# Optimization experiments

Hardware: AMD Instinct MI355X
Metric: run time of the kernel (lower is better)

## Reference

```python
import math
import jax, jax.numpy as jnp
import numpy as np


def _skew(X, pad_value):
    # shift every row i one step right relative to row i-1: [B,M,L] -> [B,M,M+L]
    B, M, L = X.shape
    X = jnp.pad(X, ((0, 0), (0, 0), (0, M + 1)), constant_values=pad_value)
    X = X.reshape(B, -1)[:, :-M]
    return X.reshape(B, M, M + L)


def _unskew(X):
    # reverse of _skew: [B,M,M+L] -> [B,M,L]
    B, M, ML = X.shape
    L = ML - M
    X = X.reshape(B, -1)
    X = jnp.pad(X, ((0, 0), (0, M)))
    X = X.reshape(B, M, M + L + 1)
    return X[:, :, :L]


def setup_inputs() -> dict:
    key0 = jax.random.key(0)
    k1, k2, k3, k4 = jax.random.split(key0, 4)
    BH, M, D = 64, 1024, 64          # batch*heads, block len, head dim
    L = 1024                          # attn_span
    return {
        "query": jax.random.normal(k1, (BH, M, D), dtype=jnp.float32),
        "key": jax.random.normal(k2, (BH, M + L, D), dtype=jnp.float32),
        "value": jax.random.normal(k3, (BH, M + L, D), dtype=jnp.float32),
        "key_pe": jax.random.normal(k4, (1, D, L), dtype=jnp.float32),
    }


def reference(query, key, value, key_pe):
    hidden_size = query.shape[-1]
    # content scores: [BH, M, M+L] -> banded [BH, M, L]
    attn_cont = _unskew(jnp.matmul(query, jnp.swapaxes(key, -1, -2)))
    # relative position scores: [BH, M, L] (key_pe broadcasts over batch)
    attn_pos = jnp.matmul(query, key_pe)
    attn = (attn_cont + attn_pos) / math.sqrt(hidden_size)
    attn = jax.nn.softmax(attn, axis=-1)
    # dropout p=0.0 -> identity
    attn_skew = _skew(attn, 0.0)          # [BH, M, M+L]
    out = jnp.matmul(attn_skew, value)    # [BH, M, D]
    return out
```

## Files before the change

### kernel.cpp

```cpp
#include <hip/hip_runtime.h>
#include <hip/hip_bf16.h>


typedef __attribute__((ext_vector_type(8))) short bf16x8;
typedef __attribute__((ext_vector_type(4))) short bf16x4;
typedef __attribute__((ext_vector_type(4))) float f32x4;

#define BHN   64
#define MQ    1024
#define DH    64
#define LS    1024
#define NKEY  2048
#define NT    18
#define NPE   16

#define SZ_PE  ((size_t)LS * DH * 2)
#define OFF_K  SZ_PE
#define SZ_K   ((size_t)BHN * NKEY * DH * 2)
#define OFF_V  (OFF_K + SZ_K)
#define SZ_V   ((size_t)BHN * DH * NKEY * 2)
#define WS_NEED (OFF_V + SZ_V)

#define SCL_LOG2E 0.18033688011112042f

__device__ __forceinline__ short f2bf(float f) {
  unsigned u = __float_as_uint(f);
  u += 0x7FFFu + ((u >> 16) & 1u);
  return (short)(u >> 16);
}
__device__ __forceinline__ float bf2f(short s) {
  return __uint_as_float(((unsigned)(unsigned short)s) << 16);
}

#if defined(__has_builtin)
#if __has_builtin(__builtin_amdgcn_cvt_pk_bf16_f32)
#define HAVE_CVT_PK 1
#endif
#if __has_builtin(__builtin_amdgcn_exp2f)
#define HAVE_EXP2 1
#endif
#endif

__device__ __forceinline__ float fast_exp2(float x) {
#ifdef HAVE_EXP2
  return __builtin_amdgcn_exp2f(x);
#else
  return __builtin_exp2f(x);
#endif
}

__device__ __forceinline__ unsigned pk2(float a, float b) {
#ifdef HAVE_CVT_PK
  auto r = __builtin_amdgcn_cvt_pk_bf16_f32(a, b);
  unsigned u;
  __builtin_memcpy(&u, &r, 4);
  return u;
#else
  return (unsigned)(unsigned short)f2bf(a) | ((unsigned)(unsigned short)f2bf(b) << 16);
#endif
}
__device__ __forceinline__ bf16x4 mk4(unsigned a, unsigned b) {
  union { unsigned u[2]; bf16x4 v; } z;
  z.u[0] = a; z.u[1] = b;
  return z.v;
}
__device__ __forceinline__ bf16x8 mk8(unsigned a, unsigned b, unsigned c, unsigned d) {
  union { unsigned u[4]; bf16x8 v; } z;
  z.u[0] = a; z.u[1] = b; z.u[2] = c; z.u[3] = d;
  return z.v;
}

__global__ __launch_bounds__(256)
void prep_fused(const float* __restrict__ pe, const float* __restrict__ K,
                const float* __restrict__ V, short* __restrict__ peT,
                short* __restrict__ Kb, short* __restrict__ Vb) {
  __shared__ short st[64 * 68];
  const int bx = blockIdx.x;
  if (bx < 256) {
    const int idx = bx * 256 + threadIdx.x;
    const int rel = idx >> 6, d = idx & 63;
    peT[rel * 64 + (((d >> 3) ^ (rel & 7)) * 8) + (d & 7)] = f2bf(pe[d * LS + rel]);
  } else if (bx < 2304) {
    const size_t i = ((size_t)(bx - 256) * 256 + threadIdx.x) * 16;
    const int row = (int)(i >> 6);
    const int c16 = (int)(i & 63);
    const float4 f0 = *(const float4*)(K + i);
    const float4 f1 = *(const float4*)(K + i + 4);
    const float4 f2 = *(const float4*)(K + i + 8);
    const float4 f3 = *(const float4*)(K + i + 12);
    const bf16x8 b0 = mk8(pk2(f0.x, f0.y), pk2(f0.z, f0.w), pk2(f1.x, f1.y), pk2(f1.z, f1.w));
    const bf16x8 b1 = mk8(pk2(f2.x, f2.y), pk2(f2.z, f2.w), pk2(f3.x, f3.y), pk2(f3.z, f3.w));
    const int s7 = row & 7;
    short* dst = Kb + (size_t)row * 64;
    *(bf16x8*)&dst[(((c16 >> 3))     ^ s7) * 8] = b0;
    *(bf16x8*)&dst[(((c16 >> 3) + 1) ^ s7) * 8] = b1;
  } else {
    const int b  = bx - 2304;
    const int bh = b >> 5, jt = b & 31;
    {
      const int r = threadIdx.x >> 2, cb = (threadIdx.x & 3) * 16;
      const float* src = V + ((size_t)bh * NKEY + jt * 64 + r) * DH + cb;
#pragma unroll
      for (int c = 0; c < 16; c += 8) {
        float4 f0 = *(const float4*)(src + c);
        float4 f1 = *(const float4*)(src + c + 4);
        *(bf16x8*)&st[r * 68 + cb + c] =
            mk8(pk2(f0.x, f0.y), pk2(f0.z, f0.w), pk2(f1.x, f1.y), pk2(f1.z, f1.w));
      }
    }
    __syncthreads();
    {
      const int d = threadIdx.x >> 2, kapb = (threadIdx.x & 3) * 16;
      __attribute__((aligned(16))) short tmp[16];
#pragma unroll
      for (int j = 0; j < 16; ++j) {
        const int kap = kapb + j;
        const int k   = (kap & 3) * 16 + (kap >> 2);
        tmp[j] = st[k * 68 + d];
      }
      short* dst = Vb + ((size_t)bh * DH + d) * NKEY + jt * 64 + kapb;
      *(bf16x8*)dst       = *(bf16x8*)&tmp[0];
      *(bf16x8*)(dst + 8) = *(bf16x8*)&tmp[8];
    }
  }
}

__device__ __forceinline__ void softmax_band(
    const f32x4* cs, const f32x4* cur, const f32x4& prev,
    float (&l_acc)[4], short* sPA, const int rowbase, const int tt,
    const int w, const int li, const int quad) {
#pragma unroll
  for (int r = 0; r < 4; ++r) {
    const int e       = li - quad * 4 - r;
    const bool ge     = (e >= 0);
    const int srcLane = quad * 16 + (e & 15);
    const float shm = __shfl(prev[r], srcLane);
    const unsigned pk01 = pk2(cur[0][r], cur[1][r]);
    const unsigned pk23 = pk2(cur[2][r], cur[3][r]);
    const unsigned s01 = (unsigned)__shfl((int)pk01, srcLane);
    const unsigned s23 = (unsigned)__shfl((int)pk23, srcLane);
    const float sh0 = bf2f((short)(s01 & 0xffffu));
    const float sh1 = bf2f((short)(s01 >> 16));
    const float sh2 = bf2f((short)(s23 & 0xffffu));
    const float sh3 = bf2f((short)(s23 >> 16));
    const float pos0 = ge ? sh0 : shm;
    const float pos1 = ge ? sh1 : sh0;
    const float pos2 = ge ? sh2 : sh1;
    const float pos3 = ge ? sh3 : sh2;
    float p0 = fast_exp2(cs[0][r] + pos0);
    float p1 = fast_exp2(cs[1][r] + pos1);
    float p2 = fast_exp2(cs[2][r] + pos2);
    float p3 = fast_exp2(cs[3][r] + pos3);
    if (tt == 0) {
      p0 = (0 > w || (0 == w && ge)) ? p0 : 0.f;
      p1 = (1 > w || (1 == w && ge)) ? p1 : 0.f;
      p2 = (2 > w || (2 == w && ge)) ? p2 : 0.f;
      p3 = (3 > w || (3 == w && ge)) ? p3 : 0.f;
    } else if (tt == 16) {
      p0 = (0 < w || (0 == w && !ge)) ? p0 : 0.f;
      p1 = (1 < w || (1 == w && !ge)) ? p1 : 0.f;
      p2 = (2 < w || (2 == w && !ge)) ? p2 : 0.f;
      p3 = (3 < w || (3 == w && !ge)) ? p3 : 0.f;
    } else if ((unsigned)tt > 16u) {
      p0 = 0.f; p1 = 0.f; p2 = 0.f; p3 = 0.f;
    }
    l_acc[r] += (p0 + p1) + (p2 + p3);
    const int rowA = rowbase + w * 16 + quad * 4 + r;
    const bf16x4 pkv = mk4(pk2(p0, p1), pk2(p2, p3));
    *(bf16x4*)&sPA[rowA * 64 + (((li >> 1) ^ (rowA & 7)) * 8) + (li & 1) * 4] = pkv;
  }
}

template <bool PRECONV>
__global__ __launch_bounds__(256, 2)
void seq_attn_kernel(const float* __restrict__ Qf, const float* __restrict__ Kf,
                     const float* __restrict__ Vf, const short* __restrict__ peT,
                     const short* __restrict__ Kb, const short* __restrict__ Vb,
                     float* __restrict__ Out) {
  __shared__ short sK[64 * 64];
  __shared__ short sPE[4 * 64 * 64];
  __shared__ short sV[64 * 64];
  __shared__ short sPA[128 * 64];

  const int tid  = threadIdx.x;
  const int w    = tid >> 6;
  const int lane = tid & 63;
  const int li   = lane & 15;
  const int quad = lane >> 4;
  const int linear = blockIdx.y * 8 + blockIdx.x;
  const int within = linear >> 3;
  const int bh     = (linear & 7) * 8 + (within >> 3);
  const int i0     = (within & 7) * 128;
  const int rbase  = w * 16 + quad * 4;

  bf16x8 aq0[2], aq1[2];
#pragma unroll
  for (int g = 0; g < 2; ++g) {
    const float* qp = Qf + (size_t)((bh * MQ + i0 + g * 64 + w * 16 + li) * DH) + quad * 8;
#pragma unroll
    for (int ks = 0; ks < 2; ++ks) {
      float4 f0 = *(const float4*)(qp + ks * 32);
      float4 f1 = *(const float4*)(qp + ks * 32 + 4);
      f0.x *= SCL_LOG2E; f0.y *= SCL_LOG2E; f0.z *= SCL_LOG2E; f0.w *= SCL_LOG2E;
      f1.x *= SCL_LOG2E; f1.y *= SCL_LOG2E; f1.z *= SCL_LOG2E; f1.w *= SCL_LOG2E;
      const bf16x8 v = mk8(pk2(f0.x, f0.y), pk2(f0.z, f0.w), pk2(f1.x, f1.y), pk2(f1.z, f1.w));
      if (g == 0) aq0[ks] = v; else aq1[ks] = v;
    }
  }

  float l0[4] = {0.f, 0.f, 0.f, 0.f};
  float l1[4] = {0.f, 0.f, 0.f, 0.f};
  f32x4 acco0[4], acco1[4];
#pragma unroll
  for (int nt = 0; nt < 4; ++nt) {
    acco0[nt] = (f32x4){0.f, 0.f, 0.f, 0.f};
    acco1[nt] = (f32x4){0.f, 0.f, 0.f, 0.f};
  }
  f32x4 prev0 = (f32x4){0.f, 0.f, 0.f, 0.f};
  f32x4 prev1 = (f32x4){0.f, 0.f, 0.f, 0.f};

  bf16x8 pfK0, pfK1, pfP0, pfP1, pfV0, pfV1;
  const short *pK, *pP, *pV0, *pV1;
  if constexpr (PRECONV) {
    pK = Kb + ((size_t)bh * NKEY + i0) * DH + tid * 8 + 1024;
    pP = peT + tid * 8 + 1024;
    const int d0 = tid >> 3;
    const int g0 = (tid & 7) ^ (d0 & 7);
    pV0 = Vb + ((size_t)bh * DH + d0) * NKEY + i0 + g0 * 8;
    pV1 = pV0 + (size_t)32 * NKEY;
    pfK0 = *(const bf16x8*)(pK - 1024);
    pfK1 = *(const bf16x8*)(pK + 1024);
    pfP0 = *(const bf16x8*)(pP - 1024);
    pfP1 = *(const bf16x8*)(pP + 1024);
    pfV0 = *(const bf16x8*)(pV0);
    pfV1 = *(const bf16x8*)(pV1);
    pK += 4096; pP += 4096; pV0 += 64; pV1 += 64;
  }

  for (int t = 0; t < NT; ++t) {
    if constexpr (PRECONV) {
      asm volatile("s_waitcnt lgkmcnt(0)" ::: "memory");
      __builtin_amdgcn_sched_barrier(0);
      __builtin_amdgcn_s_barrier();
      __builtin_amdgcn_sched_barrier(0);
      *(bf16x8*)&sK[tid * 8]        = pfK0;
      *(bf16x8*)&sK[tid * 8 + 2048] = pfK1;
      if (t < NPE) {
        short* ped = sPE + (size_t)(t & 3) * 4096;
        *(bf16x8*)&ped[tid * 8]        = pfP0;
        *(bf16x8*)&ped[tid * 8 + 2048] = pfP1;
      }
      *(bf16x8*)&sV[tid * 8]        = pfV0;
      *(bf16x8*)&sV[tid * 8 + 2048] = pfV1;
      if (t + 1 < NT) {
        pfK0 = *(const bf16x8*)(pK - 1024);
        pfK1 = *(const bf16x8*)(pK + 1024);
        pfV0 = *(const bf16x8*)(pV0);
        pfV1 = *(const bf16x8*)(pV1);
        pK += 4096; pV0 += 64; pV1 += 64;
        if (t + 1 < NPE) {
          pfP0 = *(const bf16x8*)(pP - 1024);
          pfP1 = *(const bf16x8*)(pP + 1024);
          pP += 4096;
        }
      }
      asm volatile("s_waitcnt lgkmcnt(0)" ::: "memory");
      __builtin_amdgcn_sched_barrier(0);
      __builtin_amdgcn_s_barrier();
      __builtin_amdgcn_sched_barrier(0);
    } else {
      __syncthreads();
      const int j0 = i0 + t * 64;
      {
        const int srow = tid >> 2, lx = tid & 3, sdb = lx * 16;
        const float* src = Kf + (size_t)(bh * NKEY + j0 + srow) * DH + sdb;
        const float4 a0 = *(const float4*)(src + 0);
        const float4 a1 = *(const float4*)(src + 4);
        const float4 a2 = *(const float4*)(src + 8);
        const float4 a3 = *(const float4*)(src + 12);
        const bf16x8 b0 = mk8(pk2(a0.x, a0.y), pk2(a0.z, a0.w), pk2(a1.x, a1.y), pk2(a1.z, a1.w));
        const bf16x8 b1 = mk8(pk2(a2.x, a2.y), pk2(a2.z, a2.w), pk2(a3.x, a3.y), pk2(a3.z, a3.w));
        const int s7 = srow & 7;
        *(bf16x8*)&sK[srow * 64 + (((2 * lx)     ^ s7) * 8)] = b0;
        *(bf16x8*)&sK[srow * 64 + (((2 * lx + 1) ^ s7) * 8)] = b1;
      }
      {
        const int vdb = (tid & 15) * 4, vkb = (tid >> 4) * 4;
        const float* src = Vf + (size_t)(bh * NKEY + j0 + vkb) * DH + vdb;
#pragma unroll
        for (int m = 0; m < 4; ++m) {
          const float4 rr = *(const float4*)(src + m * DH);
          const int k   = vkb + m;
          const int kap = (k & 15) * 4 + (k >> 4);
#pragma unroll
          for (int jj = 0; jj < 4; ++jj) {
            const int d = vdb + jj;
            const float fv = (jj == 0) ? rr.x : (jj == 1) ? rr.y : (jj == 2) ? rr.z : rr.w;
            sV[d * 64 + (((kap >> 3) ^ (d & 7)) * 8) + (kap & 7)] = f2bf(fv);
          }
        }
      }
      if (t < NPE) {
        const short* src = peT + (size_t)t * 64 * 64;
        short* db = sPE + (size_t)(t & 3) * 4096;
        *(bf16x8*)&db[tid * 16]     = *(const bf16x8*)(src + tid * 16);
        *(bf16x8*)&db[tid * 16 + 8] = *(const bf16x8*)(src + tid * 16 + 8);
      }
      __syncthreads();
    }

    f32x4 cur0[4], cur1[4];
    __builtin_amdgcn_s_setprio(1);
#pragma unroll
    for (int m = 0; m < 4; ++m) {
      const int colIdx = 4 * t - w + m;
      const int base = ((colIdx >> 2) & 3) * 4096 + ((colIdx & 3) * 16 + li) * 64;
      f32x4 c = (f32x4){0.f, 0.f, 0.f, 0.f};
#pragma unroll
      for (int ks = 0; ks < 2; ++ks) {
        const int gs = (((ks * 4 + quad) ^ (li & 7)) * 8);
        const bf16x8 b = *(bf16x8*)&sPE[base + gs];
        c = __builtin_amdgcn_mfma_f32_16x16x32_bf16(aq0[ks], b, c, 0, 0, 0);
      }
      cur0[m] = c;
    }
#pragma unroll
    for (int m = 0; m < 4; ++m) {
      const int colIdx = 4 * t - w + m - 4;
      const int base = ((colIdx >> 2) & 3) * 4096 + ((colIdx & 3) * 16 + li) * 64;
      f32x4 c = (f32x4){0.f, 0.f, 0.f, 0.f};
#pragma unroll
      for (int ks = 0; ks < 2; ++ks) {
        const int gs = (((ks * 4 + quad) ^ (li & 7)) * 8);
        const bf16x8 b = *(bf16x8*)&sPE[base + gs];
        c = __builtin_amdgcn_mfma_f32_16x16x32_bf16(aq1[ks], b, c, 0, 0, 0);
      }
      cur1[m] = c;
    }

    f32x4 cs0[4], cs1[4];
#pragma unroll
    for (int nt = 0; nt < 4; ++nt) {
      f32x4 c0 = (f32x4){0.f, 0.f, 0.f, 0.f};
      f32x4 c1 = (f32x4){0.f, 0.f, 0.f, 0.f};
#pragma unroll
      for (int ks = 0; ks < 2; ++ks) {
        const int gs = (((ks * 4 + quad) ^ (li & 7)) * 8);
        const bf16x8 b = *(bf16x8*)&sK[(nt * 16 + li) * 64 + gs];
        c0 = __builtin_amdgcn_mfma_f32_16x16x32_bf16(aq0[ks], b, c0, 0, 0, 0);
        c1 = __builtin_amdgcn_mfma_f32_16x16x32_bf16(aq1[ks], b, c1, 0, 0, 0);
      }
      cs0[nt] = c0; cs1[nt] = c1;
    }
    __builtin_amdgcn_s_setprio(0);

    softmax_band(cs0, cur0, prev0, l0, sPA, 0,  t,     w, li, quad);
    softmax_band(cs1, cur1, prev1, l1, sPA, 64, t - 1, w, li, quad);
    prev0 = cur0[3];
    prev1 = cur1[3];

    __builtin_amdgcn_s_setprio(1);
#pragma unroll
    for (int ks = 0; ks < 2; ++ks) {
      const int rA0 = w * 16 + li;
      const int rA1 = rA0 + 64;
      const bf16x8 ap0 = *(bf16x8*)&sPA[rA0 * 64 + (((ks * 4 + quad) ^ (rA0 & 7)) * 8)];
      const bf16x8 ap1 = *(bf16x8*)&sPA[rA1 * 64 + (((ks * 4 + quad) ^ (rA1 & 7)) * 8)];
#pragma unroll
      for (int nt = 0; nt < 4; ++nt) {
        const int d  = nt * 16 + li;
        const int gs = (((ks * 4 + quad) ^ (d & 7)) * 8);
        const bf16x8 bv = *(bf16x8*)&sV[d * 64 + gs];
        acco0[nt] = __builtin_amdgcn_mfma_f32_16x16x32_bf16(ap0, bv, acco0[nt], 0, 0, 0);
        acco1[nt] = __builtin_amdgcn_mfma_f32_16x16x32_bf16(ap1, bv, acco1[nt], 0, 0, 0);
      }
    }
    __builtin_amdgcn_s_setprio(0);
  }

#pragma unroll
  for (int r = 0; r < 4; ++r) {
    float l = l0[r];
    l += __shfl_xor(l, 1);
    l += __shfl_xor(l, 2);
    l += __shfl_xor(l, 4);
    l += __shfl_xor(l, 8);
    const float inv = 1.0f / l;
#pragma unroll
    for (int nt = 0; nt < 4; ++nt) {
      Out[(size_t)(bh * MQ + i0 + rbase + r) * DH + nt * 16 + li] = acco0[nt][r] * inv;
    }
  }
#pragma unroll
  for (int r = 0; r < 4; ++r) {
    float l = l1[r];
    l += __shfl_xor(l, 1);
    l += __shfl_xor(l, 2);
    l += __shfl_xor(l, 4);
    l += __shfl_xor(l, 8);
    const float inv = 1.0f / l;
#pragma unroll
    for (int nt = 0; nt < 4; ++nt) {
      Out[(size_t)(bh * MQ + i0 + 64 + rbase + r) * DH + nt * 16 + li] = acco1[nt][r] * inv;
    }
  }
}

extern "C" void kernel_launch(void* const* d_in, const int* in_sizes, int n_in,
                              void* d_out, int out_size, void* d_ws, size_t ws_size,
                              hipStream_t stream) {
  const float* q  = (const float*)d_in[0];
  const float* k  = (const float*)d_in[1];
  const float* v  = (const float*)d_in[2];
  const float* pe = (const float*)d_in[3];
  float* out = (float*)d_out;
  short* peT = (short*)d_ws;
  short* Kb  = (short*)((char*)d_ws + OFF_K);
  short* Vb  = (short*)((char*)d_ws + OFF_V);
  const bool preconv = ws_size >= WS_NEED;

  dim3 grid(8, BHN);
  if (preconv) {
    prep_fused<<<4352, 256, 0, stream>>>(pe, k, v, peT, Kb, Vb);
    seq_attn_kernel<true><<<grid, 256, 0, stream>>>(q, k, v, peT, Kb, Vb, out);
  } else {
    prep_fused<<<256, 256, 0, stream>>>(pe, k, v, peT, Kb, Vb);
    seq_attn_kernel<false><<<grid, 256, 0, stream>>>(q, k, v, peT, Kb, Vb, out);
  }
}
```

Before: 175.4 us.

## Shrink shared memory to fit three blocks per CU by reusing sK for P

```diff
diff --git a/kernel.cpp b/kernel.cpp
--- a/kernel.cpp
+++ b/kernel.cpp
@@ -127,7 +127,7 @@
 
 __device__ __forceinline__ void softmax_band(
     const f32x4* cs, const f32x4* cur, const f32x4& prev,
-    float (&l_acc)[4], short* sPA, const int rowbase, const int tt,
+    float (&l_acc)[4], short* dst, const int tt,
     const int w, const int li, const int quad) {
 #pragma unroll
   for (int r = 0; r < 4; ++r) {
@@ -165,22 +165,22 @@
       p0 = 0.f; p1 = 0.f; p2 = 0.f; p3 = 0.f;
     }
     l_acc[r] += (p0 + p1) + (p2 + p3);
-    const int rowA = rowbase + w * 16 + quad * 4 + r;
+    const int rowA = w * 16 + quad * 4 + r;
     const bf16x4 pkv = mk4(pk2(p0, p1), pk2(p2, p3));
-    *(bf16x4*)&sPA[rowA * 64 + (((li >> 1) ^ (rowA & 7)) * 8) + (li & 1) * 4] = pkv;
+    *(bf16x4*)&dst[rowA * 64 + (((li >> 1) ^ (rowA & 7)) * 8) + (li & 1) * 4] = pkv;
   }
 }
 
 template <bool PRECONV>
-__global__ __launch_bounds__(256, 2)
+__global__ __launch_bounds__(256, 3)
 void seq_attn_kernel(const float* __restrict__ Qf, const float* __restrict__ Kf,
                      const float* __restrict__ Vf, const short* __restrict__ peT,
                      const short* __restrict__ Kb, const short* __restrict__ Vb,
                      float* __restrict__ Out) {
   __shared__ short sK[64 * 64];
-  __shared__ short sPE[4 * 64 * 64];
+  __shared__ short sPE[3 * 64 * 64];
   __shared__ short sV[64 * 64];
-  __shared__ short sPA[128 * 64];
+  __shared__ short sPA[64 * 64];
 
   const int tid  = threadIdx.x;
   const int w    = tid >> 6;
@@ -218,6 +218,11 @@
   }
   f32x4 prev0 = (f32x4){0.f, 0.f, 0.f, 0.f};
   f32x4 prev1 = (f32x4){0.f, 0.f, 0.f, 0.f};
+
+  int peRow[4];
+#pragma unroll
+  for (int m = 0; m < 4; ++m) peRow[m] = (((m - w) & 3) * 16 + li) * 64;
+  int sCur = 0, sPrev = 2, sPrev2 = 1;
 
   bf16x8 pfK0, pfK1, pfP0, pfP1, pfV0, pfV1;
   const short *pK, *pP, *pV0, *pV1;
@@ -246,7 +251,7 @@
       *(bf16x8*)&sK[tid * 8]        = pfK0;
       *(bf16x8*)&sK[tid * 8 + 2048] = pfK1;
       if (t < NPE) {
-        short* ped = sPE + (size_t)(t & 3) * 4096;
+        short* ped = sPE + (size_t)sCur * 4096;
         *(bf16x8*)&ped[tid * 8]        = pfP0;
         *(bf16x8*)&ped[tid * 8 + 2048] = pfP1;
       }
@@ -302,7 +307,7 @@
       }
       if (t < NPE) {
         const short* src = peT + (size_t)t * 64 * 64;
-        short* db = sPE + (size_t)(t & 3) * 4096;
+        short* db = sPE + (size_t)sCur * 4096;
         *(bf16x8*)&db[tid * 16]     = *(const bf16x8*)(src + tid * 16);
         *(bf16x8*)&db[tid * 16 + 8] = *(const bf16x8*)(src + tid * 16 + 8);
       }
@@ -313,8 +318,7 @@
     __builtin_amdgcn_s_setprio(1);
 #pragma unroll
     for (int m = 0; m < 4; ++m) {
-      const int colIdx = 4 * t - w + m;
-      const int base = ((colIdx >> 2) & 3) * 4096 + ((colIdx & 3) * 16 + li) * 64;
+      const int base = ((m < w) ? sPrev : sCur) * 4096 + peRow[m];
       f32x4 c = (f32x4){0.f, 0.f, 0.f, 0.f};
 #pragma unroll
       for (int ks = 0; ks < 2; ++ks) {
@@ -326,8 +330,7 @@
     }
 #pragma unroll
     for (int m = 0; m < 4; ++m) {
-      const int colIdx = 4 * t - w + m - 4;
-      const int base = ((colIdx >> 2) & 3) * 4096 + ((colIdx & 3) * 16 + li) * 64;
+      const int base = ((m < w) ? sPrev2 : sPrev) * 4096 + peRow[m];
       f32x4 c = (f32x4){0.f, 0.f, 0.f, 0.f};
 #pragma unroll
       for (int ks = 0; ks < 2; ++ks) {
@@ -354,18 +357,24 @@
     }
     __builtin_amdgcn_s_setprio(0);
 
-    softmax_band(cs0, cur0, prev0, l0, sPA, 0,  t,     w, li, quad);
-    softmax_band(cs1, cur1, prev1, l1, sPA, 64, t - 1, w, li, quad);
+    softmax_band(cs0, cur0, prev0, l0, sPA, t,     w, li, quad);
     prev0 = cur0[3];
+
+    asm volatile("s_waitcnt lgkmcnt(0)" ::: "memory");
+    __builtin_amdgcn_sched_barrier(0);
+    __builtin_amdgcn_s_barrier();
+    __builtin_amdgcn_sched_barrier(0);
+
+    softmax_band(cs1, cur1, prev1, l1, sK, t - 1, w, li, quad);
     prev1 = cur1[3];
 
     __builtin_amdgcn_s_setprio(1);
 #pragma unroll
     for (int ks = 0; ks < 2; ++ks) {
-      const int rA0 = w * 16 + li;
-      const int rA1 = rA0 + 64;
-      const bf16x8 ap0 = *(bf16x8*)&sPA[rA0 * 64 + (((ks * 4 + quad) ^ (rA0 & 7)) * 8)];
-      const bf16x8 ap1 = *(bf16x8*)&sPA[rA1 * 64 + (((ks * 4 + quad) ^ (rA1 & 7)) * 8)];
+      const int rA = w * 16 + li;
+      const int psw = (((ks * 4 + quad) ^ (rA & 7)) * 8);
+      const bf16x8 ap0 = *(bf16x8*)&sPA[rA * 64 + psw];
+      const bf16x8 ap1 = *(bf16x8*)&sK[rA * 64 + psw];
 #pragma unroll
       for (int nt = 0; nt < 4; ++nt) {
         const int d  = nt * 16 + li;
@@ -376,6 +385,9 @@
       }
     }
     __builtin_amdgcn_s_setprio(0);
+
+    const int sNew = sPrev2;
+    sPrev2 = sPrev; sPrev = sCur; sCur = sNew;
   }
 
 #pragma unroll
```

After: 245.6 us. 1.4x slower.
